# Optimization experiments

Hardware: AMD Instinct MI355X
Metric: run time of the kernel (lower is better)

Reference implementation:

```python
import jax, jax.numpy as jnp
import numpy as np

N_NODES = 100000
N_EDGES = 1600000
D_IN = 64
D_OUT = 64


def setup_inputs() -> dict:
    key = jax.random.key(0)
    k1, k2, k3, k4 = jax.random.split(key, 4)
    features = jax.random.normal(k1, (N_NODES, D_IN), dtype=jnp.float32)
    src = jax.random.randint(k2, (N_EDGES,), 0, N_NODES, dtype=jnp.int32)
    dst = jax.random.randint(k3, (N_EDGES,), 0, N_NODES, dtype=jnp.int32)
    # nn.Linear(input_dim, output_dim): W is [out, in], bias [out]
    W = jax.random.normal(k4, (D_OUT, D_IN), dtype=jnp.float32) * (1.0 / np.sqrt(D_IN))
    b = jnp.zeros((D_OUT,), dtype=jnp.float32)
    return {"features": features, "src": src, "dst": dst, "W": W, "b": b}


def reference(features, src, dst, W, b):
    # DGL update_all(copy_src('h'), sum('m')): for each node v, h[v] = sum over
    # in-edges (u -> v) of features[u].  Gather at src, segment-sum at dst.
    msgs = features[src]  # [E, D_in]
    agg = jax.ops.segment_sum(msgs, dst, num_segments=features.shape[0])  # [N, D_in]
    # nn.Linear: agg @ W.T + b
    return agg @ W.T + b
```

## Files before the change

kernel.cpp:

```cpp
#include <hip/hip_runtime.h>

#define NN 100000
#define NE 1600000
#define D 64
#define BKT_SHIFT 7
#define BKT_NODES 128
#define BKT_MASK 127
#define NBKT 782
#define SRC_MASK 0x1FFFF
#define EPB 8192
#define NPB ((NE + EPB - 1) / EPB)
#define BINCAP 2560
#define HCAP 1600
#define TROWS 16
#define NTILE (NN / TROWS)
#define TGRID 2048

__device__ __forceinline__ unsigned short f2bf(float f) {
    unsigned u = __float_as_uint(f);
    unsigned r = u + 0x7FFF + ((u >> 16) & 1);
    return (unsigned short)(r >> 16);
}

__device__ __forceinline__ int cmp4(const int4& v, int k) {
    return k == 0 ? v.x : k == 1 ? v.y : k == 2 ? v.z : v.w;
}

__global__ __launch_bounds__(256) void seed_cursor(int* __restrict__ cursor) {
    const int i = blockIdx.x * 256 + threadIdx.x;
    if (i < NBKT) cursor[i] = 0;
}

__global__ __launch_bounds__(256) void fused_tp2(const float* __restrict__ feat,
                                                 const float* __restrict__ W,
                                                 unsigned short* __restrict__ hb,
                                                 const int* __restrict__ src,
                                                 const int* __restrict__ dst,
                                                 int* __restrict__ cursor,
                                                 int* __restrict__ binned) {
    __shared__ int hist[NBKT];
    __shared__ float4 rowLds[TROWS][16];
    const int t = threadIdx.x;

    if (blockIdx.x < NPB) {
        for (int i = t; i < NBKT; i += 256) hist[i] = 0;
        __syncthreads();

        const int4* __restrict__ src4 = (const int4*)src;
        const int4* __restrict__ dst4 = (const int4*)dst;
        const int qlo = blockIdx.x * (EPB / 4);
        const int nq  = NE / 4;

        int4 dv[8];
        int  rk[8][4];
#pragma unroll
        for (int it = 0; it < 8; ++it) {
            const int idx = qlo + it * 256 + t;
            dv[it] = (idx < nq) ? dst4[idx] : make_int4(-1, -1, -1, -1);
        }
#pragma unroll
        for (int it = 0; it < 8; ++it)
#pragma unroll
            for (int k = 0; k < 4; ++k) {
                const int d = cmp4(dv[it], k);
                if (d >= 0) rk[it][k] = atomicAdd(&hist[d >> BKT_SHIFT], 1);
            }
        __syncthreads();

        for (int i = t; i < NBKT; i += 256) {
            const int c = hist[i];
            int base = i * BINCAP;
            if (c) base += atomicAdd(&cursor[i], c);
            hist[i] = base;
        }
        __syncthreads();

#pragma unroll
        for (int it = 0; it < 8; ++it) {
            const int idx = qlo + it * 256 + t;
            if (idx < nq) {
                const int4 s4 = src4[idx];
#pragma unroll
                for (int k = 0; k < 4; ++k) {
                    const int d = cmp4(dv[it], k);
                    const int s = cmp4(s4, k);
                    binned[hist[d >> BKT_SHIFT] + rk[it][k]] =
                        s | ((d & BKT_MASK) << 17);
                }
            }
        }
    } else {
        const int bid  = blockIdx.x - NPB;
        const int lane = t & 63;
        const int wv   = t >> 6;
        float4 wreg[16];
        const float4* __restrict__ W4 = (const float4*)W;
#pragma unroll
        for (int i = 0; i < 16; ++i) wreg[i] = W4[lane * 16 + i];

        for (int tile = bid; tile < NTILE; tile += TGRID) {
            const int rowBase = tile * TROWS;
            rowLds[t >> 4][t & 15] =
                ((const float4*)(feat + (size_t)(rowBase + (t >> 4)) * D))[t & 15];
            __syncthreads();
            float a0 = 0.f, a1 = 0.f, a2 = 0.f, a3 = 0.f;
#pragma unroll
            for (int k4 = 0; k4 < 16; ++k4) {
                const float4 w  = wreg[k4];
                const float4 r0 = rowLds[wv * 4 + 0][k4];
                const float4 r1 = rowLds[wv * 4 + 1][k4];
                const float4 r2 = rowLds[wv * 4 + 2][k4];
                const float4 r3 = rowLds[wv * 4 + 3][k4];
                a0 += r0.x * w.x + r0.y * w.y + r0.z * w.z + r0.w * w.w;
                a1 += r1.x * w.x + r1.y * w.y + r1.z * w.z + r1.w * w.w;
                a2 += r2.x * w.x + r2.y * w.y + r2.z * w.z + r2.w * w.w;
                a3 += r3.x * w.x + r3.y * w.y + r3.z * w.z + r3.w * w.w;
            }
            const size_t ob = (size_t)(rowBase + wv * 4) * D + lane;
            hb[ob]         = f2bf(a0);
            hb[ob + D]     = f2bf(a1);
            hb[ob + 2 * D] = f2bf(a2);
            hb[ob + 3 * D] = f2bf(a3);
            __syncthreads();
        }
    }
}

__global__ __launch_bounds__(256) void bucket_gather(const uint2* __restrict__ hb2,
                                                     const int* __restrict__ binned,
                                                     const int* __restrict__ cursor,
                                                     const float* __restrict__ bias,
                                                     float4* __restrict__ out4) {
    __shared__ int cnt[64];
    __shared__ int pre[64];
    __shared__ int sEdge[HCAP];
    const int t = threadIdx.x;
    const int b = blockIdx.x >> 1;
    const int h = blockIdx.x & 1;
    if (t < 64) cnt[t] = 0;
    __syncthreads();

    const int gbase = b * BINCAP;
    int sz = cursor[b];
    if (sz > BINCAP) sz = BINCAP;

    int pk[10], dd[10], rr[10];
#pragma unroll
    for (int it = 0; it < 10; ++it) {
        const int e = it * 256 + t;
        dd[it] = -1;
        if (e < sz) {
            const int p = binned[gbase + e];
            const int d7 = (p >> 17) & BKT_MASK;
            if ((d7 >> 6) == h) {
                dd[it] = d7 & 63;
                pk[it] = p & SRC_MASK;
                rr[it] = atomicAdd(&cnt[dd[it]], 1);
            }
        }
    }
    __syncthreads();

    if (t < 64) {
        int v = cnt[t];
#pragma unroll
        for (int s = 1; s < 64; s <<= 1) {
            const int u = __shfl_up(v, s);
            if (t >= s) v += u;
        }
        pre[t] = v;
    }
    __syncthreads();

#pragma unroll
    for (int it = 0; it < 10; ++it) {
        if (dd[it] >= 0) {
            const int pos = pre[dd[it]] - cnt[dd[it]] + rr[it];
            if (pos < HCAP) sEdge[pos] = pk[it];
        }
    }
    __syncthreads();

    const int q  = t >> 4;
    const int c4 = t & 15;
    const float4 bv = ((const float4*)bias)[c4];
#pragma unroll
    for (int i = 0; i < 4; ++i) {
        const int n    = q * 4 + i;
        const int node = b * BKT_NODES + h * 64 + n;
        if (node >= NN) break;
        int end = pre[n];
        if (end > HCAP) end = HCAP;
        int e = end - cnt[n];
        if (e < 0) e = 0;
        float ax = 0.f, ay = 0.f, az = 0.f, aw = 0.f;
        for (; e < end; e += 8) {
            uint2 x[8];
#pragma unroll
            for (int j = 0; j < 8; ++j) {
                const int idx = (e + j < end) ? sEdge[e + j] : -1;
                x[j] = (idx >= 0) ? hb2[(size_t)idx * 16 + c4] : make_uint2(0u, 0u);
            }
#pragma unroll
            for (int j = 0; j < 8; ++j) {
                ax += __uint_as_float(x[j].x << 16);
                ay += __uint_as_float(x[j].x & 0xFFFF0000u);
                az += __uint_as_float(x[j].y << 16);
                aw += __uint_as_float(x[j].y & 0xFFFF0000u);
            }
        }
        float4 v;
        v.x = ax + bv.x; v.y = ay + bv.y; v.z = az + bv.z; v.w = aw + bv.w;
        out4[(size_t)node * 16 + c4] = v;
    }
}

extern "C" void kernel_launch(void* const* d_in, const int* in_sizes, int n_in,
                              void* d_out, int out_size, void* d_ws, size_t ws_size,
                              hipStream_t stream) {
    const float* feat = (const float*)d_in[0];
    const int*   src  = (const int*)d_in[1];
    const int*   dst  = (const int*)d_in[2];
    const float* W    = (const float*)d_in[3];
    const float* bias = (const float*)d_in[4];
    float4* out = (float4*)d_out;

    unsigned short* hb = (unsigned short*)d_ws;
    int* binned = (int*)(hb + (size_t)NN * D);
    int* cursor = binned + NBKT * BINCAP;

    seed_cursor<<<(NBKT + 255) / 256, 256, 0, stream>>>(cursor);
    fused_tp2<<<NPB + TGRID, 256, 0, stream>>>(feat, W, hb, src, dst, cursor, binned);
    bucket_gather<<<2 * NBKT, 256, 0, stream>>>((const uint2*)hb, binned, cursor,
                                                bias, out);
}
```

Measured before the change: 153.1 us.

## Replace LDS-staged transform tiles with per-wave readlane broadcast and prefetch

The feature-times-W transform no longer stages 16 rows in shared memory with block-wide barriers. Each wavefront now loads its own 4 rows (one float4 per lane) and broadcasts row elements to all lanes with readlane, which removes both __syncthreads per tile. It also software-prefetches the next tile's row data while computing the current one. The cost is 64 scalar readlane operations per tile, which go through the scalar path and may limit throughput.

```diff
diff --git a/kernel.cpp b/kernel.cpp
--- a/kernel.cpp
+++ b/kernel.cpp
@@ -12,8 +12,7 @@
 #define NPB ((NE + EPB - 1) / EPB)
 #define BINCAP 2560
 #define HCAP 1600
-#define TROWS 16
-#define NTILE (NN / TROWS)
+#define NT4 (NN / 4)
 #define TGRID 2048
 
 __device__ __forceinline__ unsigned short f2bf(float f) {
@@ -24,6 +23,10 @@
 
 __device__ __forceinline__ int cmp4(const int4& v, int k) {
     return k == 0 ? v.x : k == 1 ? v.y : k == 2 ? v.z : v.w;
+}
+
+__device__ __forceinline__ float rl(float v, int sl) {
+    return __uint_as_float(__builtin_amdgcn_readlane(__float_as_uint(v), sl));
 }
 
 __global__ __launch_bounds__(256) void seed_cursor(int* __restrict__ cursor) {
@@ -39,7 +42,6 @@
                                                  int* __restrict__ cursor,
                                                  int* __restrict__ binned) {
     __shared__ int hist[NBKT];
-    __shared__ float4 rowLds[TROWS][16];
     const int t = threadIdx.x;
 
     if (blockIdx.x < NPB) {
@@ -97,31 +99,42 @@
         const float4* __restrict__ W4 = (const float4*)W;
 #pragma unroll
         for (int i = 0; i < 16; ++i) wreg[i] = W4[lane * 16 + i];
-
-        for (int tile = bid; tile < NTILE; tile += TGRID) {
-            const int rowBase = tile * TROWS;
-            rowLds[t >> 4][t & 15] =
-                ((const float4*)(feat + (size_t)(rowBase + (t >> 4)) * D))[t & 15];
-            __syncthreads();
-            float a0 = 0.f, a1 = 0.f, a2 = 0.f, a3 = 0.f;
-#pragma unroll
-            for (int k4 = 0; k4 < 16; ++k4) {
-                const float4 w  = wreg[k4];
-                const float4 r0 = rowLds[wv * 4 + 0][k4];
-                const float4 r1 = rowLds[wv * 4 + 1][k4];
-                const float4 r2 = rowLds[wv * 4 + 2][k4];
-                const float4 r3 = rowLds[wv * 4 + 3][k4];
-                a0 += r0.x * w.x + r0.y * w.y + r0.z * w.z + r0.w * w.w;
-                a1 += r1.x * w.x + r1.y * w.y + r1.z * w.z + r1.w * w.w;
-                a2 += r2.x * w.x + r2.y * w.y + r2.z * w.z + r2.w * w.w;
-                a3 += r3.x * w.x + r3.y * w.y + r3.z * w.z + r3.w * w.w;
-            }
-            const size_t ob = (size_t)(rowBase + wv * 4) * D + lane;
-            hb[ob]         = f2bf(a0);
-            hb[ob + D]     = f2bf(a1);
-            hb[ob + 2 * D] = f2bf(a2);
-            hb[ob + 3 * D] = f2bf(a3);
-            __syncthreads();
+        const float4* __restrict__ F4 = (const float4*)feat;
+
+        const int wid  = bid * 4 + wv;
+        const int wstr = TGRID * 4;
+
+        int tcur = wid;
+        if (tcur < NT4) {
+            float4 cur = F4[(size_t)tcur * 64 + lane];
+            for (;;) {
+                const int tnxt = tcur + wstr;
+                float4 nxt = make_float4(0.f, 0.f, 0.f, 0.f);
+                if (tnxt < NT4) nxt = F4[(size_t)tnxt * 64 + lane];
+
+                float a0 = 0.f, a1 = 0.f, a2 = 0.f, a3 = 0.f;
+#pragma unroll
+                for (int k4 = 0; k4 < 16; ++k4) {
+                    const float4 w = wreg[k4];
+                    a0 += rl(cur.x, k4)      * w.x + rl(cur.y, k4)      * w.y
+                        + rl(cur.z, k4)      * w.z + rl(cur.w, k4)      * w.w;
+                    a1 += rl(cur.x, 16 + k4) * w.x + rl(cur.y, 16 + k4) * w.y
+                        + rl(cur.z, 16 + k4) * w.z + rl(cur.w, 16 + k4) * w.w;
+                    a2 += rl(cur.x, 32 + k4) * w.x + rl(cur.y, 32 + k4) * w.y
+                        + rl(cur.z, 32 + k4) * w.z + rl(cur.w, 32 + k4) * w.w;
+                    a3 += rl(cur.x, 48 + k4) * w.x + rl(cur.y, 48 + k4) * w.y
+                        + rl(cur.z, 48 + k4) * w.z + rl(cur.w, 48 + k4) * w.w;
+                }
+                const size_t ob = (size_t)tcur * 4 * D + lane;
+                hb[ob]         = f2bf(a0);
+                hb[ob + D]     = f2bf(a1);
+                hb[ob + 2 * D] = f2bf(a2);
+                hb[ob + 3 * D] = f2bf(a3);
+
+                if (tnxt >= NT4) break;
+                cur = nxt;
+                tcur = tnxt;
+            }
         }
     }
 }
```

Result: slower. 158.1 us (+3.3%).
